# Kernel tuning notes

Hardware: AMD Instinct MI355X
Metric: run time of the kernel (lower is better)

Reference implementation:

```python
import jax, jax.numpy as jnp
import numpy as np

B, S, D = 4, 2048, 1024
H, DK, DV = 16, 64, 64


def setup_inputs() -> dict:
    key = jax.random.key(0)
    ks = jax.random.split(key, 7)
    scale = 0.02
    emb = jax.random.normal(ks[0], (B, S, D), dtype=jnp.float32)
    # per-head projection weights stacked over heads: [H, D, DK/DV]
    Wq = jax.random.normal(ks[1], (H, D, DK), dtype=jnp.float32) * scale
    Wk = jax.random.normal(ks[2], (H, D, DK), dtype=jnp.float32) * scale
    Wv = jax.random.normal(ks[3], (H, D, DV), dtype=jnp.float32) * scale
    # output projection (nn.Linear(d_model, d_model)): weight [D, D] (input-major) + bias
    Wo = jax.random.normal(ks[4], (D, D), dtype=jnp.float32) * scale
    bo = jax.random.normal(ks[5], (D,), dtype=jnp.float32) * scale
    return {"emb": emb, "Wq": Wq, "Wk": Wk, "Wv": Wv, "Wo": Wo, "bo": bo}


def reference(emb, Wq, Wk, Wv, Wo, bo):
    # Per-head projections, batched over heads: [B,H,S,dk]
    q = jnp.einsum("bsd,hdk->bhsk", emb, Wq)
    k = jnp.einsum("bsd,hdk->bhsk", emb, Wk)
    v = jnp.einsum("bsd,hdv->bhsv", emb, Wv)
    # Scaled dot-product with causal mask (bool_mask=True)
    scores = jnp.einsum("bhqk,bhsk->bhqs", q, k) * (DK ** -0.5)  # [B,H,S,S]
    causal = jnp.tril(jnp.ones((S, S), dtype=bool))
    scores = jnp.where(causal, scores, jnp.finfo(scores.dtype).min)
    attn = jax.nn.softmax(scores, axis=-1)
    out = jnp.einsum("bhqs,bhsv->bhqv", attn, v)  # [B,H,S,DV]
    # concat heads -> [B,S,H*DV] == [B,S,D]
    out = out.transpose(0, 2, 1, 3).reshape(B, S, H * DV)
    # output projection; dropout=0.0 -> identity
    return out @ Wo + bo
```

## Files before the change

### kernel.cpp

```cpp
#include <hip/hip_runtime.h>
#include <hip/hip_bf16.h>


typedef __attribute__((ext_vector_type(8))) short bf16x8;
typedef __attribute__((ext_vector_type(4))) float f32x4;
typedef __attribute__((ext_vector_type(4))) unsigned int u32x4;
typedef __attribute__((ext_vector_type(2))) unsigned int u32x2;

#define MFMA16(a, b, c) __builtin_amdgcn_mfma_f32_16x16x32_bf16((a), (b), (c), 0, 0, 0)

#define LOG2E 1.44269504088896340736f
#define BIG_NEG (-3.0e38f)
#define DEFER_THR 10.0f

__device__ __forceinline__ unsigned short f2bf(float f) {
  union { float f; unsigned int i; } x; x.f = f;
  unsigned int lsb = (x.i >> 16) & 1;
  x.i += 0x7fffu + lsb;
  return (unsigned short)(x.i >> 16);
}

__device__ __forceinline__ unsigned int cvtpk(float lo, float hi) {
  unsigned int r;
  asm("v_cvt_pk_bf16_f32 %0, %1, %2" : "=v"(r) : "v"(lo), "v"(hi));
  return r;
}

__global__ void wtrans_kernel(const float* __restrict__ in,
                              unsigned short* __restrict__ out, int R, int C) {
  __shared__ unsigned short tile[32][33];
  const int bz = blockIdx.z;
  const int c0 = blockIdx.x * 32, r0 = blockIdx.y * 32;
  const float* ip = in + (size_t)bz * R * C;
  unsigned short* op = out + (size_t)bz * R * C;
  const int tx = threadIdx.x, ty = threadIdx.y;
#pragma unroll
  for (int i = 0; i < 32; i += 8)
    tile[ty + i][tx] = f2bf(ip[(size_t)(r0 + ty + i) * C + (c0 + tx)]);
  __syncthreads();
#pragma unroll
  for (int i = 0; i < 32; i += 8)
    op[(size_t)(c0 + ty + i) * R + (r0 + tx)] = tile[tx][ty + i];
}

__global__ __launch_bounds__(256)
void embconv_kernel(const float* __restrict__ in, unsigned short* __restrict__ out) {
  const int i = blockIdx.x * 256 + threadIdx.x;
  const float4 a = ((const float4*)in)[2 * i];
  const float4 b = ((const float4*)in)[2 * i + 1];
  union { unsigned short u[8]; u32x4 v; } p;
  p.u[0] = f2bf(a.x); p.u[1] = f2bf(a.y); p.u[2] = f2bf(a.z); p.u[3] = f2bf(a.w);
  p.u[4] = f2bf(b.x); p.u[5] = f2bf(b.y); p.u[6] = f2bf(b.z); p.u[7] = f2bf(b.w);
  ((u32x4*)out)[i] = p.v;
}

__global__ __launch_bounds__(256)
void qkv_kernel(const unsigned short* __restrict__ embB,
                const unsigned short* __restrict__ WqT,
                const unsigned short* __restrict__ WkT,
                const unsigned short* __restrict__ WvT,
                unsigned short* __restrict__ QG,
                unsigned short* __restrict__ KG,
                unsigned short* __restrict__ VtG) {
  const int t = blockIdx.z;
  const int m0 = blockIdx.y * 128;
  const int n0 = blockIdx.x * 128;
  const int b = m0 >> 11;
  const int sloc = m0 & 2047;
  const unsigned short* Wt =
      (t == 0 ? WqT : (t == 1 ? WkT : WvT)) + (size_t)(n0 >> 6) * 64 * 1024;

  __shared__ __align__(16) unsigned short As[128][40];
  __shared__ __align__(16) unsigned short Bs[128][40];

  const int tid = threadIdx.x;
  const int lane = tid & 63, w = tid >> 6;
  const int q4 = lane >> 4, l16 = lane & 15;
  const int arow = tid >> 1, acol = (tid & 1) * 16;

  f32x4 acc[4][4] = {};

  for (int k0 = 0; k0 < 1024; k0 += 32) {
    __syncthreads();
    *(u32x4*)&As[arow][acol]     = *(const u32x4*)&embB[(size_t)(m0 + arow) * 1024 + k0 + acol];
    *(u32x4*)&As[arow][acol + 8] = *(const u32x4*)&embB[(size_t)(m0 + arow) * 1024 + k0 + acol + 8];
    *(u32x4*)&Bs[arow][acol]     = *(const u32x4*)&Wt[(size_t)arow * 1024 + k0 + acol];
    *(u32x4*)&Bs[arow][acol + 8] = *(const u32x4*)&Wt[(size_t)arow * 1024 + k0 + acol + 8];
    __syncthreads();

    const unsigned short (*PA)[40] = (t == 2) ? Bs : As;
    const unsigned short (*PB)[40] = (t == 2) ? As : Bs;

    bf16x8 af[4], bfr[4];
#pragma unroll
    for (int ms = 0; ms < 4; ++ms)
      af[ms] = *(const bf16x8*)&PA[(w >> 1) * 64 + ms * 16 + l16][q4 * 8];
#pragma unroll
    for (int js = 0; js < 4; ++js)
      bfr[js] = *(const bf16x8*)&PB[(w & 1) * 64 + js * 16 + l16][q4 * 8];
#pragma unroll
    for (int ms = 0; ms < 4; ++ms)
#pragma unroll
      for (int js = 0; js < 4; ++js)
        acc[ms][js] = MFMA16(af[ms], bfr[js], acc[ms][js]);
  }

  if (t < 2) {
    unsigned short* outp = (t == 0) ? QG : KG;
    const float osc = (t == 0) ? (0.125f * LOG2E) : 1.0f;
    const int h = (n0 >> 6) + (w & 1);
    const size_t hb = (size_t)(b * 16 + h) * 2048;
#pragma unroll
    for (int ms = 0; ms < 4; ++ms)
#pragma unroll
      for (int js = 0; js < 4; ++js) {
        const int c = js * 16 + l16;
#pragma unroll
        for (int r = 0; r < 4; ++r) {
          const int s = sloc + (w >> 1) * 64 + ms * 16 + q4 * 4 + r;
          outp[(hb + s) * 64 + c] = f2bf(acc[ms][js][r] * osc);
        }
      }
  } else {
    const int h = (n0 >> 6) + (w >> 1);
    const size_t hb = (size_t)(b * 16 + h) * 64;
#pragma unroll
    for (int ms = 0; ms < 4; ++ms)
#pragma unroll
      for (int js = 0; js < 4; ++js) {
        const int s = sloc + (w & 1) * 64 + js * 16 + l16;
#pragma unroll
        for (int r = 0; r < 4; ++r) {
          const int c = ms * 16 + q4 * 4 + r;
          VtG[(hb + c) * 2048 + s] = f2bf(acc[ms][js][r]);
        }
      }
  }
}

__global__ __launch_bounds__(512)
void flash_kernel(const unsigned short* __restrict__ QG,
                  const unsigned short* __restrict__ KG,
                  const unsigned short* __restrict__ VtG,
                  unsigned short* __restrict__ ObG) {
  const int bh = blockIdx.y;
  const int x = blockIdx.x;
  const int q0B = (31 - x) * 64;
  const int tid = threadIdx.x;
  const int lane = tid & 63, w = tid >> 6;
  const int wp = w & 3;
  const int q0w = (w < 4) ? q0B : x * 64;
  const int q4 = lane >> 4, l16 = lane & 15;

  const unsigned short* Qp = QG + ((size_t)bh * 2048 + q0w + wp * 16) * 64;
  const unsigned short* Kp = KG + (size_t)bh * 2048 * 64;
  const unsigned short* Vp = VtG + (size_t)bh * 64 * 2048;

  const bf16x8 qf0 = *(const bf16x8*)&Qp[(size_t)l16 * 64 + q4 * 8];
  const bf16x8 qf1 = *(const bf16x8*)&Qp[(size_t)l16 * 64 + 32 + q4 * 8];

  __shared__ __align__(16) unsigned short Ks[64][72];
  __shared__ __align__(16) unsigned short Vs[64][72];
  __shared__ __align__(16) unsigned short Plds[8][16][72];

  f32x4 oacc[4] = {};
  float m_i = BIG_NEG, l_i = 0.f;

  const int sr = tid >> 3, sc = (tid & 7) * 8;
  u32x4 kreg = *(const u32x4*)&Kp[(size_t)sr * 64 + sc];
  u32x4 vreg = *(const u32x4*)&Vp[(size_t)sr * 2048 + sc];

  for (int j0 = 0; j0 <= q0B; j0 += 64) {
    *(u32x4*)&Ks[sr][sc] = kreg;
    *(u32x4*)&Vs[sr][sc] = vreg;
    __syncthreads();

    if (j0 + 64 <= q0B) {
      const int jn = j0 + 64;
      kreg = *(const u32x4*)&Kp[(size_t)(jn + sr) * 64 + sc];
      vreg = *(const u32x4*)&Vp[(size_t)sr * 2048 + jn + sc];
    }

    if (j0 <= q0w) {
      f32x4 sacc[4] = {};
#pragma unroll
      for (int js = 0; js < 4; ++js) {
        const bf16x8 kf0 = *(const bf16x8*)&Ks[js * 16 + l16][q4 * 8];
        const bf16x8 kf1 = *(const bf16x8*)&Ks[js * 16 + l16][32 + q4 * 8];
        sacc[js] = MFMA16(kf0, qf0, sacc[js]);
        sacc[js] = MFMA16(kf1, qf1, sacc[js]);
      }

      float mloc = BIG_NEG;
      if (j0 == q0w) {
        const int qrel = wp * 16 + l16;
#pragma unroll
        for (int js = 0; js < 4; ++js)
#pragma unroll
          for (int r = 0; r < 4; ++r) {
            const int krel = js * 16 + q4 * 4 + r;
            float v = sacc[js][r];
            if (krel > qrel) v = BIG_NEG;
            sacc[js][r] = v;
            mloc = fmaxf(mloc, v);
          }
      } else {
#pragma unroll
        for (int js = 0; js < 4; ++js)
#pragma unroll
          for (int r = 0; r < 4; ++r) mloc = fmaxf(mloc, sacc[js][r]);
      }
      mloc = fmaxf(mloc, __shfl_xor(mloc, 16, 64));
      mloc = fmaxf(mloc, __shfl_xor(mloc, 32, 64));

      if (__any(mloc > m_i + DEFER_THR)) {
        const float mnew = fmaxf(m_i, mloc);
        const float alpha = __builtin_amdgcn_exp2f(m_i - mnew);
        m_i = mnew;
        l_i *= alpha;
#pragma unroll
        for (int js = 0; js < 4; ++js)
#pragma unroll
          for (int r = 0; r < 4; ++r) oacc[js][r] *= alpha;
      }

      float sm = 0.f;
#pragma unroll
      for (int js = 0; js < 4; ++js)
#pragma unroll
        for (int r = 0; r < 4; ++r) {
          const float p = __builtin_amdgcn_exp2f(sacc[js][r] - m_i);
          sacc[js][r] = p;
          sm += p;
        }
      sm += __shfl_xor(sm, 16, 64);
      sm += __shfl_xor(sm, 32, 64);
      l_i += sm;

#pragma unroll
      for (int js = 0; js < 4; ++js) {
        u32x2 pk;
        pk[0] = cvtpk(sacc[js][0], sacc[js][1]);
        pk[1] = cvtpk(sacc[js][2], sacc[js][3]);
        *(u32x2*)&Plds[w][l16][js * 16 + q4 * 4] = pk;
      }

      asm volatile("" ::: "memory");

      const bf16x8 pf0 = *(const bf16x8*)&Plds[w][l16][q4 * 8];
      const bf16x8 pf1 = *(const bf16x8*)&Plds[w][l16][32 + q4 * 8];

#pragma unroll
      for (int js = 0; js < 4; ++js) {
        const bf16x8 vf0 = *(const bf16x8*)&Vs[js * 16 + l16][q4 * 8];
        const bf16x8 vf1 = *(const bf16x8*)&Vs[js * 16 + l16][32 + q4 * 8];
        oacc[js] = MFMA16(vf0, pf0, oacc[js]);
        oacc[js] = MFMA16(vf1, pf1, oacc[js]);
      }
    }
    __syncthreads();
  }

  const int b = bh >> 4, h = bh & 15;
  const int q = q0w + wp * 16 + l16;
  const float rl = 1.0f / l_i;
  unsigned short* orow = ObG + ((size_t)b * 2048 + q) * 1024 + h * 64;
#pragma unroll
  for (int js = 0; js < 4; ++js) {
    u32x2 ok;
    ok[0] = cvtpk(oacc[js][0] * rl, oacc[js][1] * rl);
    ok[1] = cvtpk(oacc[js][2] * rl, oacc[js][3] * rl);
    *(u32x2*)&orow[js * 16 + q4 * 4] = ok;
  }
}

__global__ __launch_bounds__(256)
void oproj_kernel(const unsigned short* __restrict__ ObG,
                  const unsigned short* __restrict__ WoT,
                  const float* __restrict__ bo,
                  float* __restrict__ outG) {
  const int m0 = blockIdx.y * 128;
  const int n0 = blockIdx.x * 128;

  __shared__ __align__(16) unsigned short As[128][40];
  __shared__ __align__(16) unsigned short Bs[128][40];

  const int tid = threadIdx.x;
  const int lane = tid & 63, w = tid >> 6;
  const int q4 = lane >> 4, l16 = lane & 15;
  const int arow = tid >> 1, acol = (tid & 1) * 16;

  f32x4 acc[4][4] = {};

  for (int k0 = 0; k0 < 1024; k0 += 32) {
    __syncthreads();
    *(u32x4*)&As[arow][acol]     = *(const u32x4*)&ObG[(size_t)(m0 + arow) * 1024 + k0 + acol];
    *(u32x4*)&As[arow][acol + 8] = *(const u32x4*)&ObG[(size_t)(m0 + arow) * 1024 + k0 + acol + 8];
    *(u32x4*)&Bs[arow][acol]     = *(const u32x4*)&WoT[(size_t)(n0 + arow) * 1024 + k0 + acol];
    *(u32x4*)&Bs[arow][acol + 8] = *(const u32x4*)&WoT[(size_t)(n0 + arow) * 1024 + k0 + acol + 8];
    __syncthreads();

    bf16x8 af[4], bfr[4];
#pragma unroll
    for (int ms = 0; ms < 4; ++ms)
      af[ms] = *(const bf16x8*)&As[(w >> 1) * 64 + ms * 16 + l16][q4 * 8];
#pragma unroll
    for (int js = 0; js < 4; ++js)
      bfr[js] = *(const bf16x8*)&Bs[(w & 1) * 64 + js * 16 + l16][q4 * 8];
#pragma unroll
    for (int ms = 0; ms < 4; ++ms)
#pragma unroll
      for (int js = 0; js < 4; ++js)
        acc[ms][js] = MFMA16(af[ms], bfr[js], acc[ms][js]);
  }

#pragma unroll
  for (int js = 0; js < 4; ++js) {
    const int col = n0 + (w & 1) * 64 + js * 16 + l16;
    const float bias = bo[col];
#pragma unroll
    for (int ms = 0; ms < 4; ++ms)
#pragma unroll
      for (int r = 0; r < 4; ++r) {
        const int row = m0 + (w >> 1) * 64 + ms * 16 + q4 * 4 + r;
        outG[(size_t)row * 1024 + col] = acc[ms][js][r] + bias;
      }
  }
}

extern "C" void kernel_launch(void* const* d_in, const int* in_sizes, int n_in,
                              void* d_out, int out_size, void* d_ws, size_t ws_size,
                              hipStream_t stream) {
  const float* emb = (const float*)d_in[0];
  const float* Wq  = (const float*)d_in[1];
  const float* Wk  = (const float*)d_in[2];
  const float* Wv  = (const float*)d_in[3];
  const float* Wo  = (const float*)d_in[4];
  const float* bo  = (const float*)d_in[5];
  float* out = (float*)d_out;

  char* ws = (char*)d_ws;
  const size_t MB = 1024 * 1024;

  const int nb = (ws_size >= 72 * MB) ? 4 : (ws_size >= 40 * MB) ? 2 : 1;

  unsigned short* WqT = (unsigned short*)(ws + 0 * MB);
  unsigned short* WkT = (unsigned short*)(ws + 2 * MB);
  unsigned short* WvT = (unsigned short*)(ws + 4 * MB);
  unsigned short* WoT = (unsigned short*)(ws + 6 * MB);
  unsigned short* QG  = (unsigned short*)(ws + 8 * MB);
  unsigned short* KG  = (unsigned short*)(ws + (8 + 4 * nb) * MB);
  unsigned short* VtG = (unsigned short*)(ws + (8 + 8 * nb) * MB);
  unsigned short* ObG = (unsigned short*)(ws + (8 + 12 * nb) * MB);

  const dim3 tb(32, 8, 1);
  wtrans_kernel<<<dim3(2, 32, 16), tb, 0, stream>>>(Wq, WqT, 1024, 64);
  wtrans_kernel<<<dim3(2, 32, 16), tb, 0, stream>>>(Wk, WkT, 1024, 64);
  wtrans_kernel<<<dim3(2, 32, 16), tb, 0, stream>>>(Wv, WvT, 1024, 64);
  wtrans_kernel<<<dim3(32, 32, 1), tb, 0, stream>>>(Wo, WoT, 1024, 1024);

  for (int g = 0; g < 4; g += nb) {
    const float* embG = emb + (size_t)g * 2048 * 1024;
    float* outG = out + (size_t)g * 2048 * 1024;
    unsigned short* embB = ObG;
    embconv_kernel<<<dim3(nb * 1024), 256, 0, stream>>>(embG, embB);
    qkv_kernel<<<dim3(8, 16 * nb, 3), 256, 0, stream>>>(embB, WqT, WkT, WvT, QG, KG, VtG);
    flash_kernel<<<dim3(16, 16 * nb), 512, 0, stream>>>(QG, KG, VtG, ObG);
    oproj_kernel<<<dim3(8, 16 * nb), 256, 0, stream>>>(ObG, WoT, bo, outG);
  }
}
```

Before: 304.3 us.

## Use direct global-to-LDS loads, XCD block swizzle, and MFMA priority hints

The GEMM kernels now stage tiles with global_load_lds (direct global-to-LDS DMA) into unpadded 32-wide LDS tiles instead of loading into registers and then storing to LDS. Block indices are swizzled so consecutive workgroups land on the same XCD region, aiming for better L2 reuse. The flash grid is transposed so heads vary fastest. s_setprio is wrapped around the MFMA sections. Removing the LDS padding may bring back bank conflicts on the fragment reads, and the swizzle assumes the block count divides by 8.

```diff
diff --git a/kernel.cpp b/kernel.cpp
--- a/kernel.cpp
+++ b/kernel.cpp
@@ -24,6 +24,12 @@
   unsigned int r;
   asm("v_cvt_pk_bf16_f32 %0, %1, %2" : "=v"(r) : "v"(lo), "v"(hi));
   return r;
+}
+
+__device__ __forceinline__ void gl16(const unsigned short* g, void* l) {
+  __builtin_amdgcn_global_load_lds(
+      (const __attribute__((address_space(1))) unsigned int*)g,
+      (__attribute__((address_space(3))) unsigned int*)l, 16, 0, 0);
 }
 
 __global__ void wtrans_kernel(const float* __restrict__ in,
@@ -62,47 +68,61 @@
                 unsigned short* __restrict__ QG,
                 unsigned short* __restrict__ KG,
                 unsigned short* __restrict__ VtG) {
-  const int t = blockIdx.z;
-  const int m0 = blockIdx.y * 128;
-  const int n0 = blockIdx.x * 128;
+  const int nwg = gridDim.x;
+  const int wg = blockIdx.x;
+  const int swz = (wg & 7) * (nwg >> 3) + (wg >> 3);
+  const int mb = swz / 24;
+  const int rem = swz - mb * 24;
+  const int t = rem >> 3;
+  const int m0 = mb * 128;
+  const int n0 = (rem & 7) * 128;
   const int b = m0 >> 11;
   const int sloc = m0 & 2047;
   const unsigned short* Wt =
       (t == 0 ? WqT : (t == 1 ? WkT : WvT)) + (size_t)(n0 >> 6) * 64 * 1024;
 
-  __shared__ __align__(16) unsigned short As[128][40];
-  __shared__ __align__(16) unsigned short Bs[128][40];
+  __shared__ __align__(16) unsigned short As[128 * 32];
+  __shared__ __align__(16) unsigned short Bs[128 * 32];
 
   const int tid = threadIdx.x;
   const int lane = tid & 63, w = tid >> 6;
   const int q4 = lane >> 4, l16 = lane & 15;
-  const int arow = tid >> 1, acol = (tid & 1) * 16;
+  const int lr = lane >> 2, lc = (lane & 3) * 8;
 
   f32x4 acc[4][4] = {};
 
+  const unsigned short* ga0 = &embB[(size_t)(m0 + w * 32 + lr) * 1024 + lc];
+  const unsigned short* ga1 = ga0 + 16 * 1024;
+  const unsigned short* gb0 = &Wt[(size_t)(w * 32 + lr) * 1024 + lc];
+  const unsigned short* gb1 = gb0 + 16 * 1024;
+  char* la0 = (char*)As + w * 2048;
+  char* lb0 = (char*)Bs + w * 2048;
+
   for (int k0 = 0; k0 < 1024; k0 += 32) {
     __syncthreads();
-    *(u32x4*)&As[arow][acol]     = *(const u32x4*)&embB[(size_t)(m0 + arow) * 1024 + k0 + acol];
-    *(u32x4*)&As[arow][acol + 8] = *(const u32x4*)&embB[(size_t)(m0 + arow) * 1024 + k0 + acol + 8];
-    *(u32x4*)&Bs[arow][acol]     = *(const u32x4*)&Wt[(size_t)arow * 1024 + k0 + acol];
-    *(u32x4*)&Bs[arow][acol + 8] = *(const u32x4*)&Wt[(size_t)arow * 1024 + k0 + acol + 8];
-    __syncthreads();
-
-    const unsigned short (*PA)[40] = (t == 2) ? Bs : As;
-    const unsigned short (*PB)[40] = (t == 2) ? As : Bs;
+    gl16(ga0 + k0, la0);
+    gl16(ga1 + k0, la0 + 1024);
+    gl16(gb0 + k0, lb0);
+    gl16(gb1 + k0, lb0 + 1024);
+    __syncthreads();
+
+    const unsigned short* PA = (t == 2) ? Bs : As;
+    const unsigned short* PB = (t == 2) ? As : Bs;
 
     bf16x8 af[4], bfr[4];
 #pragma unroll
     for (int ms = 0; ms < 4; ++ms)
-      af[ms] = *(const bf16x8*)&PA[(w >> 1) * 64 + ms * 16 + l16][q4 * 8];
+      af[ms] = *(const bf16x8*)&PA[((w >> 1) * 64 + ms * 16 + l16) * 32 + q4 * 8];
 #pragma unroll
     for (int js = 0; js < 4; ++js)
-      bfr[js] = *(const bf16x8*)&PB[(w & 1) * 64 + js * 16 + l16][q4 * 8];
+      bfr[js] = *(const bf16x8*)&PB[((w & 1) * 64 + js * 16 + l16) * 32 + q4 * 8];
+    __builtin_amdgcn_s_setprio(1);
 #pragma unroll
     for (int ms = 0; ms < 4; ++ms)
 #pragma unroll
       for (int js = 0; js < 4; ++js)
         acc[ms][js] = MFMA16(af[ms], bfr[js], acc[ms][js]);
+    __builtin_amdgcn_s_setprio(0);
   }
 
   if (t < 2) {
@@ -143,8 +163,8 @@
                   const unsigned short* __restrict__ KG,
                   const unsigned short* __restrict__ VtG,
                   unsigned short* __restrict__ ObG) {
-  const int bh = blockIdx.y;
-  const int x = blockIdx.x;
+  const int bh = blockIdx.x;
+  const int x = blockIdx.y;
   const int q0B = (31 - x) * 64;
   const int tid = threadIdx.x;
   const int lane = tid & 63, w = tid >> 6;
@@ -183,6 +203,7 @@
 
     if (j0 <= q0w) {
       f32x4 sacc[4] = {};
+      __builtin_amdgcn_s_setprio(1);
 #pragma unroll
       for (int js = 0; js < 4; ++js) {
         const bf16x8 kf0 = *(const bf16x8*)&Ks[js * 16 + l16][q4 * 8];
@@ -190,6 +211,7 @@
         sacc[js] = MFMA16(kf0, qf0, sacc[js]);
         sacc[js] = MFMA16(kf1, qf1, sacc[js]);
       }
+      __builtin_amdgcn_s_setprio(0);
 
       float mloc = BIG_NEG;
       if (j0 == q0w) {
@@ -250,6 +272,7 @@
       const bf16x8 pf0 = *(const bf16x8*)&Plds[w][l16][q4 * 8];
       const bf16x8 pf1 = *(const bf16x8*)&Plds[w][l16][32 + q4 * 8];
 
+      __builtin_amdgcn_s_setprio(1);
 #pragma unroll
       for (int js = 0; js < 4; ++js) {
         const bf16x8 vf0 = *(const bf16x8*)&Vs[js * 16 + l16][q4 * 8];
@@ -257,6 +280,7 @@
         oacc[js] = MFMA16(vf0, pf0, oacc[js]);
         oacc[js] = MFMA16(vf1, pf1, oacc[js]);
       }
+      __builtin_amdgcn_s_setprio(0);
     }
     __syncthreads();
   }
@@ -279,39 +303,51 @@
                   const unsigned short* __restrict__ WoT,
                   const float* __restrict__ bo,
                   float* __restrict__ outG) {
-  const int m0 = blockIdx.y * 128;
-  const int n0 = blockIdx.x * 128;
-
-  __shared__ __align__(16) unsigned short As[128][40];
-  __shared__ __align__(16) unsigned short Bs[128][40];
+  const int nwg = gridDim.x;
+  const int wg = blockIdx.x;
+  const int swz = (wg & 7) * (nwg >> 3) + (wg >> 3);
+  const int m0 = (swz >> 3) * 128;
+  const int n0 = (swz & 7) * 128;
+
+  __shared__ __align__(16) unsigned short As[128 * 32];
+  __shared__ __align__(16) unsigned short Bs[128 * 32];
 
   const int tid = threadIdx.x;
   const int lane = tid & 63, w = tid >> 6;
   const int q4 = lane >> 4, l16 = lane & 15;
-  const int arow = tid >> 1, acol = (tid & 1) * 16;
+  const int lr = lane >> 2, lc = (lane & 3) * 8;
 
   f32x4 acc[4][4] = {};
 
+  const unsigned short* ga0 = &ObG[(size_t)(m0 + w * 32 + lr) * 1024 + lc];
+  const unsigned short* ga1 = ga0 + 16 * 1024;
+  const unsigned short* gb0 = &WoT[(size_t)(n0 + w * 32 + lr) * 1024 + lc];
+  const unsigned short* gb1 = gb0 + 16 * 1024;
+  char* la0 = (char*)As + w * 2048;
+  char* lb0 = (char*)Bs + w * 2048;
+
   for (int k0 = 0; k0 < 1024; k0 += 32) {
     __syncthreads();
-    *(u32x4*)&As[arow][acol]     = *(const u32x4*)&ObG[(size_t)(m0 + arow) * 1024 + k0 + acol];
-    *(u32x4*)&As[arow][acol + 8] = *(const u32x4*)&ObG[(size_t)(m0 + arow) * 1024 + k0 + acol + 8];
-    *(u32x4*)&Bs[arow][acol]     = *(const u32x4*)&WoT[(size_t)(n0 + arow) * 1024 + k0 + acol];
-    *(u32x4*)&Bs[arow][acol + 8] = *(const u32x4*)&WoT[(size_t)(n0 + arow) * 1024 + k0 + acol + 8];
+    gl16(ga0 + k0, la0);
+    gl16(ga1 + k0, la0 + 1024);
+    gl16(gb0 + k0, lb0);
+    gl16(gb1 + k0, lb0 + 1024);
     __syncthreads();
 
     bf16x8 af[4], bfr[4];
 #pragma unroll
     for (int ms = 0; ms < 4; ++ms)
-      af[ms] = *(const bf16x8*)&As[(w >> 1) * 64 + ms * 16 + l16][q4 * 8];
+      af[ms] = *(const bf16x8*)&As[((w >> 1) * 64 + ms * 16 + l16) * 32 + q4 * 8];
 #pragma unroll
     for (int js = 0; js < 4; ++js)
-      bfr[js] = *(const bf16x8*)&Bs[(w & 1) * 64 + js * 16 + l16][q4 * 8];
+      bfr[js] = *(const bf16x8*)&Bs[((w & 1) * 64 + js * 16 + l16) * 32 + q4 * 8];
+    __builtin_amdgcn_s_setprio(1);
 #pragma unroll
     for (int ms = 0; ms < 4; ++ms)
 #pragma unroll
       for (int js = 0; js < 4; ++js)
         acc[ms][js] = MFMA16(af[ms], bfr[js], acc[ms][js]);
+    __builtin_amdgcn_s_setprio(0);
   }
 
 #pragma unroll
@@ -364,8 +400,8 @@
     float* outG = out + (size_t)g * 2048 * 1024;
     unsigned short* embB = ObG;
     embconv_kernel<<<dim3(nb * 1024), 256, 0, stream>>>(embG, embB);
-    qkv_kernel<<<dim3(8, 16 * nb, 3), 256, 0, stream>>>(embB, WqT, WkT, WvT, QG, KG, VtG);
-    flash_kernel<<<dim3(16, 16 * nb), 512, 0, stream>>>(QG, KG, VtG, ObG);
-    oproj_kernel<<<dim3(8, 16 * nb), 256, 0, stream>>>(ObG, WoT, bo, outG);
-  }
-}
+    qkv_kernel<<<dim3(24 * 16 * nb), 256, 0, stream>>>(embB, WqT, WkT, WvT, QG, KG, VtG);
+    flash_kernel<<<dim3(16 * nb, 16), 512, 0, stream>>>(QG, KG, VtG, ObG);
+    oproj_kernel<<<dim3(8 * 16 * nb), 256, 0, stream>>>(ObG, WoT, bo, outG);
+  }
+}
```

Measured after the change: 282.5 us. 7.2% less time.
